# Performance work log

Measured on AMD Instinct MI355X. Metric: run time of the kernel, lower is better.

Reference implementation:

```python
import jax, jax.numpy as jnp
import numpy as np

DIM = 1024
NUM_HEADS = 16
DIM_PER_HEAD = 64
INNER = NUM_HEADS * DIM_PER_HEAD  # 1024
SCALE = DIM_PER_HEAD ** -0.5
EPS = 1e-10


def setup_inputs() -> dict:
    key = jax.random.key(0)
    k_x, k_m, k_qkv, k_wo, k_bo = jax.random.split(key, 5)
    b, l = 2, 2048
    x = jax.random.normal(k_x, (b, l, DIM), dtype=jnp.float32)
    # binary multiplicative mask [b, l, l]
    mask = jax.random.randint(k_m, (b, l, l), 0, 2).astype(jnp.float32)
    # nn.Linear(dim, 3*inner, bias=False): weight [3*inner, dim]; we store transposed [dim, 3*inner]
    W_qkv = jax.random.normal(k_qkv, (DIM, 3 * INNER), dtype=jnp.float32) * (DIM ** -0.5)
    W_out = jax.random.normal(k_wo, (INNER, DIM), dtype=jnp.float32) * (INNER ** -0.5)
    b_out = jax.random.normal(k_bo, (DIM,), dtype=jnp.float32) * 0.01
    return {"x": x, "mask": mask, "W_qkv": W_qkv, "W_out": W_out, "b_out": b_out}


def reference(x, mask, W_qkv, W_out, b_out):
    b, l, d = x.shape
    qkv = x @ W_qkv  # [b, l, 3*inner]
    qkv = qkv.reshape(b, l, 3, NUM_HEADS, DIM_PER_HEAD)
    qkv = jnp.transpose(qkv, (2, 0, 3, 1, 4))  # [3, b, h, l, dh]
    q, k, v = qkv[0], qkv[1], qkv[2]
    # softmax FIRST (no additive mask), matching the original module
    attn = jax.nn.softmax(jnp.einsum('bhid,bhjd->bhij', q, k) * SCALE, axis=-1)  # [b,h,l,l]
    # multiplicative mask then renormalize
    attn = attn * mask[:, None, :, :]
    attn = attn / (jnp.sum(attn, axis=-1, keepdims=True) + EPS)
    z = jnp.einsum('bhij,bhjd->bhid', attn, v)  # [b,h,l,dh]
    z = jnp.transpose(z, (0, 2, 1, 3)).reshape(b, l, INNER)
    out = z @ W_out + b_out  # dropout p=0 -> identity
    return out
```

## Files before the change

### kernel.cpp

```cpp
#include <hip/hip_runtime.h>
#include <hip/hip_bf16.h>

#define BATCH 2
#define SEQ   2048
#define DIM   1024
#define HEADS 16
#define DH    64
#define N_QKV 3072
#define M_TOT 4096
#define SCALE 0.125f
#define EPS   1e-10f
#define LOG2E 1.442695041f

typedef __attribute__((ext_vector_type(8))) _Float16 half8;
typedef __attribute__((ext_vector_type(4))) float f32x4;

static __device__ __forceinline__ unsigned short f2h(float f) {
    _Float16 h = (_Float16)f;
    return __builtin_bit_cast(unsigned short, h);
}
static __device__ __forceinline__ unsigned int pkrtz(float a, float b) {
#if defined(__has_builtin) && __has_builtin(__builtin_amdgcn_cvt_pkrtz)
    return __builtin_bit_cast(unsigned int, __builtin_amdgcn_cvt_pkrtz(a, b));
#else
    return (unsigned int)f2h(a) | ((unsigned int)f2h(b) << 16);
#endif
}
static __device__ __forceinline__ void glds16(const void* g, void* l) {
    __builtin_amdgcn_global_load_lds((const __attribute__((address_space(1))) void*)g,
                                     (__attribute__((address_space(3))) void*)l,
                                     16, 0, 0);
}

__global__ __launch_bounds__(256) void prepass(const float* __restrict__ x,
                                               unsigned short* __restrict__ xh,
                                               const float* __restrict__ Wq,
                                               unsigned short* __restrict__ WqT,
                                               const float* __restrict__ Wo,
                                               unsigned short* __restrict__ WoT,
                                               const float* __restrict__ mask,
                                               unsigned short* __restrict__ mbits) {
    const int bid = blockIdx.x;
    const int t   = threadIdx.x;
    __shared__ float tile[32][33];
    __shared__ unsigned char flags[16][256];

    if (bid < 4096) {
        const int i = bid * 256 + t;
        float4 v = reinterpret_cast<const float4*>(x)[i];
        uint2 o;
        o.x = pkrtz(v.x, v.y);
        o.y = pkrtz(v.z, v.w);
        reinterpret_cast<uint2*>(xh)[i] = o;
    } else if (bid < 8192) {
        const float* src; unsigned short* th; int rows, cols, bx;
        if (bid < 7168) { src = Wq; th = WqT; rows = 1024; cols = 3072; bx = bid - 4096;
        } else          { src = Wo; th = WoT; rows = 1024; cols = 1024; bx = bid - 7168; }
        const int nbx = cols / 32;
        const int c0 = (bx % nbx) * 32, r0 = (bx / nbx) * 32;
        const int tx = t & 31, ty = t >> 5;
        #pragma unroll
        for (int i = ty; i < 32; i += 8)
            tile[i][tx] = src[(long)(r0 + i) * cols + c0 + tx];
        __syncthreads();
        #pragma unroll
        for (int i = ty; i < 32; i += 8)
            th[(long)(c0 + i) * rows + r0 + tx] = f2h(tile[tx][i]);
    } else {
        const int bx = bid - 8192;
        const int it = bx & 127;
        const int bb = bx >> 7;
        const int R0 = it * 16;
        const int tl = t >> 6, ln = t & 63;
        for (int c0 = 0; c0 < SEQ; c0 += 256) {
            #pragma unroll
            for (int rr = 0; rr < 16; ++rr)
                flags[rr][t] = mask[((long)bb * SEQ + R0 + rr) * SEQ + c0 + t] != 0.f;
            __syncthreads();
            unsigned int bits = 0;
            #pragma unroll
            for (int nt = 0; nt < 4; ++nt)
                #pragma unroll
                for (int r = 0; r < 4; ++r)
                    bits |= (unsigned int)flags[ln & 15][tl * 64 + nt * 16 + ((ln >> 4) << 2) + r]
                            << (nt * 4 + r);
            mbits[(((long)bb * 128 + it) * 32 + (c0 >> 6) + tl) * 64 + ln] = (unsigned short)bits;
            __syncthreads();
        }
    }
}

__global__ __launch_bounds__(256, 3) void gemm_qkv_f16(
    const unsigned short* __restrict__ Ahg, const unsigned short* __restrict__ Bhg,
    unsigned short* __restrict__ qb, unsigned short* __restrict__ kb,
    unsigned short* __restrict__ vtb) {
    __shared__ __align__(16) unsigned short As[128 * 64];
    __shared__ __align__(16) unsigned short Bs[128 * 64];

    const int n0   = blockIdx.x * 128;
    const int m0   = blockIdx.y * 128;
    const int wave = threadIdx.x >> 6;
    const int lane = threadIdx.x & 63;
    const int l16  = lane & 15;
    const int g    = lane >> 4;
    const int wm   = wave & 1;
    const int wn   = wave >> 1;
    const int sw   = l16 & 7;

    const int sr8 = lane >> 3;
    const int scg = (lane & 7) ^ sr8;

    f32x4 acc[4][4] = {};

    for (int k0 = 0; k0 < DIM; k0 += 64) {
        #pragma unroll
        for (int i = 0; i < 4; ++i) {
            const int row = wave * 32 + i * 8;
            glds16(Ahg + (long)(m0 + row + sr8) * DIM + k0 + scg * 8, &As[row * 64]);
            glds16(Bhg + (long)(n0 + row + sr8) * DIM + k0 + scg * 8, &Bs[row * 64]);
        }
        __syncthreads();

        #pragma unroll
        for (int kc = 0; kc < 2; ++kc) {
            half8 a[4], b[4];
            #pragma unroll
            for (int mt = 0; mt < 4; ++mt)
                a[mt] = *reinterpret_cast<const half8*>(
                    &As[(wm * 64 + mt * 16 + l16) * 64 + (((kc * 4 + g) ^ sw) * 8)]);
            #pragma unroll
            for (int nt = 0; nt < 4; ++nt)
                b[nt] = *reinterpret_cast<const half8*>(
                    &Bs[(wn * 64 + nt * 16 + l16) * 64 + (((kc * 4 + g) ^ sw) * 8)]);
            #pragma unroll
            for (int mt = 0; mt < 4; ++mt)
                #pragma unroll
                for (int nt = 0; nt < 4; ++nt)
                    acc[mt][nt] = __builtin_amdgcn_mfma_f32_16x16x32_f16(
                        a[mt], b[nt], acc[mt][nt], 0, 0, 0);
        }
        __syncthreads();
    }

    #pragma unroll
    for (int nt = 0; nt < 4; ++nt) {
        const int n     = n0 + wn * 64 + nt * 16 + l16;
        const int which = n >> 10;
        const int rem   = n & 1023;
        const int head  = rem >> 6;
        const int d     = rem & 63;
        #pragma unroll
        for (int mt = 0; mt < 4; ++mt) {
            #pragma unroll
            for (int r = 0; r < 4; ++r) {
                const int m  = m0 + wm * 64 + mt * 16 + g * 4 + r;
                const int bb = m >> 11;
                const int li = m & 2047;
                const int bh_i = bb * HEADS + head;
                const float val = acc[mt][nt][r];
                if (which == 0)
                    qb[((long)bh_i * SEQ + li) * DH + d] = f2h(val * (SCALE * LOG2E));
                else if (which == 1)
                    kb[((long)bh_i * SEQ + li) * DH + d] = f2h(val);
                else
                    vtb[((long)bh_i * DH + d) * SEQ + li] = f2h(val);
            }
        }
    }
}

__global__ __launch_bounds__(256, 4) void gemm_out_f16(
    const unsigned short* __restrict__ Ahg, const unsigned short* __restrict__ Bhg,
    const float* __restrict__ bias, float* __restrict__ out) {
    __shared__ __align__(16) unsigned short As[64 * 64];
    __shared__ __align__(16) unsigned short Bs[64 * 64];

    const int n0   = blockIdx.x * 64;
    const int m0   = blockIdx.y * 64;
    const int wave = threadIdx.x >> 6;
    const int lane = threadIdx.x & 63;
    const int l16  = lane & 15;
    const int g    = lane >> 4;
    const int wm   = wave & 1;
    const int wn   = wave >> 1;
    const int sw   = l16 & 7;

    const int sr8 = lane >> 3;
    const int scg = (lane & 7) ^ sr8;

    f32x4 acc[2][2] = {};

    for (int k0 = 0; k0 < DIM; k0 += 64) {
        #pragma unroll
        for (int i = 0; i < 2; ++i) {
            const int row = wave * 16 + i * 8;
            glds16(Ahg + (long)(m0 + row + sr8) * DIM + k0 + scg * 8, &As[row * 64]);
            glds16(Bhg + (long)(n0 + row + sr8) * DIM + k0 + scg * 8, &Bs[row * 64]);
        }
        __syncthreads();

        half8 a[2][2];
        #pragma unroll
        for (int mt = 0; mt < 2; ++mt) {
            const int rbase = (wm * 32 + mt * 16 + l16) * 64;
            #pragma unroll
            for (int kc = 0; kc < 2; ++kc)
                a[mt][kc] = *reinterpret_cast<const half8*>(
                    &As[rbase + (((kc * 4 + g) ^ sw) * 8)]);
        }
        #pragma unroll
        for (int nt = 0; nt < 2; ++nt) {
            const int rbase = (wn * 32 + nt * 16 + l16) * 64;
            const half8 b0 = *reinterpret_cast<const half8*>(&Bs[rbase + (((0 + g) ^ sw) * 8)]);
            const half8 b1 = *reinterpret_cast<const half8*>(&Bs[rbase + (((4 + g) ^ sw) * 8)]);
            #pragma unroll
            for (int mt = 0; mt < 2; ++mt) {
                acc[mt][nt] = __builtin_amdgcn_mfma_f32_16x16x32_f16(a[mt][0], b0, acc[mt][nt], 0, 0, 0);
                acc[mt][nt] = __builtin_amdgcn_mfma_f32_16x16x32_f16(a[mt][1], b1, acc[mt][nt], 0, 0, 0);
            }
        }
        __syncthreads();
    }

    #pragma unroll
    for (int nt = 0; nt < 2; ++nt) {
        const int n  = n0 + wn * 32 + nt * 16 + l16;
        const float bv = bias[n];
        #pragma unroll
        for (int mt = 0; mt < 2; ++mt) {
            #pragma unroll
            for (int r = 0; r < 4; ++r) {
                const int m = m0 + wm * 32 + mt * 16 + g * 4 + r;
                out[(long)m * DIM + n] = acc[mt][nt][r] + bv;
            }
        }
    }
}

__global__ __launch_bounds__(512, 6) void attn_mfma(const unsigned short* __restrict__ qb,
                                                    const unsigned short* __restrict__ kb,
                                                    const unsigned short* __restrict__ vtb,
                                                    const unsigned short* __restrict__ mbits,
                                                    unsigned short* __restrict__ zh) {
    const int qt   = blockIdx.x;
    const int h    = blockIdx.y;
    const int bb   = blockIdx.z;
    const int bh   = bb * HEADS + h;
    const int wave = threadIdx.x >> 6;
    const int lane = threadIdx.x & 63;
    const int l16  = lane & 15;
    const int g    = lane >> 4;
    const int wm   = wave >> 1;
    const int wj   = wave & 1;

    const int myrow0 = qt * 64 + wm * 16;

    __shared__ __align__(16) unsigned short KV[2][2][64 * 64];
    __shared__ __align__(16) unsigned short Ps[8][16 * 64];

    const int sr8 = lane >> 3;
    const int scg = (lane & 7) ^ sr8;
    const int sw  = l16 & 7;

    const unsigned short* qptr = qb + ((long)bh * SEQ + myrow0 + l16) * DH + g * 8;
    const half8 q0 = *reinterpret_cast<const half8*>(qptr);
    const half8 q1 = *reinterpret_cast<const half8*>(qptr + 32);

    half8 ones;
    #pragma unroll
    for (int j = 0; j < 8; ++j) ones[j] = (_Float16)1.0f;

    f32x4 o[4] = {};
    f32x4 oz = {0.f, 0.f, 0.f, 0.f};

    const unsigned short* mb =
        mbits + (((long)bb * 128 + qt * 4 + wm) * 32 + wj * 16) * 64 + lane;
    const long kbase = (long)bh * SEQ * DH;
    const long vbase = (long)bh * DH * SEQ;
    const int  jb    = wj * 1024;

    for (int it = 0; it < 16; ++it) {
        const int j0 = jb + it * 64;
        const unsigned int bits = mb[(long)it * 64];

        #pragma unroll
        for (int i = 0; i < 2; ++i) {
            const int row = wm * 16 + i * 8;
            glds16(kb  + kbase + (long)(j0 + row + sr8) * DH + scg * 8, &KV[wj][0][row * 64]);
            glds16(vtb + vbase + (long)(row + sr8) * SEQ + j0 + scg * 8, &KV[wj][1][row * 64]);
        }
        __syncthreads();

        f32x4 st[4];
        #pragma unroll
        for (int nt = 0; nt < 4; ++nt) {
            const int rbase = (nt * 16 + l16) * 64;
            const half8 k0 = *reinterpret_cast<const half8*>(&KV[wj][0][rbase + ((0 + g) ^ sw) * 8]);
            const half8 k1 = *reinterpret_cast<const half8*>(&KV[wj][0][rbase + (((4 + g) ^ sw) * 8)]);
            f32x4 acc = {0.f, 0.f, 0.f, 0.f};
            acc = __builtin_amdgcn_mfma_f32_16x16x32_f16(k0, q0, acc, 0, 0, 0);
            acc = __builtin_amdgcn_mfma_f32_16x16x32_f16(k1, q1, acc, 0, 0, 0);
            st[nt] = acc;
        }

        #pragma unroll
        for (int nt = 0; nt < 4; ++nt) {
            float pm[4];
            #pragma unroll
            for (int r = 0; r < 4; ++r) {
                const float p = __builtin_amdgcn_exp2f(st[nt][r]);
                pm[r] = ((bits >> (nt * 4 + r)) & 1u) ? p : 0.f;
            }
            uint2 pk;
            pk.x = pkrtz(pm[0], pm[1]);
            pk.y = pkrtz(pm[2], pm[3]);
            *reinterpret_cast<uint2*>(
                &Ps[wave][l16 * 64 + (((2 * nt + (g >> 1)) ^ sw) * 8) + (g & 1) * 4]) = pk;
        }

        const half8 pb0 = *reinterpret_cast<const half8*>(&Ps[wave][l16 * 64 + ((0 + g) ^ sw) * 8]);
        const half8 pb1 = *reinterpret_cast<const half8*>(&Ps[wave][l16 * 64 + (((4 + g) ^ sw) * 8)]);
        #pragma unroll
        for (int dt = 0; dt < 4; ++dt) {
            const int vb = (dt * 16 + l16) * 64;
            const half8 v0 = *reinterpret_cast<const half8*>(&KV[wj][1][vb + ((0 + g) ^ sw) * 8]);
            const half8 v1 = *reinterpret_cast<const half8*>(&KV[wj][1][vb + (((4 + g) ^ sw) * 8)]);
            o[dt] = __builtin_amdgcn_mfma_f32_16x16x32_f16(v0, pb0, o[dt], 0, 0, 0);
            o[dt] = __builtin_amdgcn_mfma_f32_16x16x32_f16(v1, pb1, o[dt], 0, 0, 0);
        }
        oz = __builtin_amdgcn_mfma_f32_16x16x32_f16(ones, pb0, oz, 0, 0, 0);
        oz = __builtin_amdgcn_mfma_f32_16x16x32_f16(ones, pb1, oz, 0, 0, 0);
        __syncthreads();
    }

    float* cmb = (float*)&KV[0][0][0];
    const int ci = wm * 16 + l16;
    if (wj == 1) {
        #pragma unroll
        for (int dt = 0; dt < 4; ++dt)
            *reinterpret_cast<f32x4*>(&cmb[ci * 68 + dt * 16 + g * 4]) = o[dt];
        if (g == 0) cmb[4352 + ci] = oz[0];
    }
    __syncthreads();
    if (wj == 0) {
        const float Z   = oz[0] + cmb[4352 + ci];
        const float inv = 1.f / (Z + 1e-30f);
        const long obase = ((long)bb * SEQ + myrow0 + l16) * DIM + h * DH;
        #pragma unroll
        for (int dt = 0; dt < 4; ++dt) {
            const f32x4 oc = *reinterpret_cast<const f32x4*>(&cmb[ci * 68 + dt * 16 + g * 4]);
            uint2 pk;
            pk.x = pkrtz((o[dt][0] + oc[0]) * inv, (o[dt][1] + oc[1]) * inv);
            pk.y = pkrtz((o[dt][2] + oc[2]) * inv, (o[dt][3] + oc[3]) * inv);
            *reinterpret_cast<uint2*>(zh + obase + dt * 16 + g * 4) = pk;
        }
    }
}

extern "C" void kernel_launch(void* const* d_in, const int* in_sizes, int n_in,
                              void* d_out, int out_size, void* d_ws, size_t ws_size,
                              hipStream_t stream) {
    const float* x     = (const float*)d_in[0];
    const float* mask  = (const float*)d_in[1];
    const float* W_qkv = (const float*)d_in[2];
    const float* W_out = (const float*)d_in[3];
    const float* b_out = (const float*)d_in[4];
    float* out = (float*)d_out;

    unsigned short* ws = (unsigned short*)d_ws;
    unsigned short* xh    = ws;
    unsigned short* WqT   = xh    + 4194304;
    unsigned short* WoT   = WqT   + 3145728;
    unsigned short* qbu   = WoT   + 1048576;
    unsigned short* kbu   = qbu   + 4194304;
    unsigned short* vtb   = kbu   + 4194304;
    unsigned short* mbits = vtb   + 4194304;
    unsigned short* zz    = xh;

    prepass<<<8448, 256, 0, stream>>>(x, xh, W_qkv, WqT, W_out, WoT, mask, mbits);

    gemm_qkv_f16<<<dim3(24, 32), 256, 0, stream>>>(xh, WqT, qbu, kbu, vtb);

    attn_mfma<<<dim3(SEQ / 64, HEADS, BATCH), 512, 0, stream>>>(qbu, kbu, vtb, mbits, zz);

    gemm_out_f16<<<dim3(16, 64), 256, 0, stream>>>(zz, WoT, b_out, out);
}
```

Baseline: 229.4 us.

## Process 128 query rows per attention block to reuse K/V tiles

The attention kernel now handles 128 query rows per block instead of 64. Each wave computes two 16-row query sub-tiles against the same K/V tiles loaded into shared memory, which halves global K/V traffic and the number of barriers per query row. The cost is more registers per wave (the launch-bounds occupancy hint drops from 6 to 4), a larger shared memory footprint, and half as many blocks in the grid.

```diff
diff --git a/kernel.cpp b/kernel.cpp
--- a/kernel.cpp
+++ b/kernel.cpp
@@ -237,7 +237,7 @@
     }
 }
 
-__global__ __launch_bounds__(512, 6) void attn_mfma(const unsigned short* __restrict__ qb,
+__global__ __launch_bounds__(512, 4) void attn_mfma(const unsigned short* __restrict__ qb,
                                                     const unsigned short* __restrict__ kb,
                                                     const unsigned short* __restrict__ vtb,
                                                     const unsigned short* __restrict__ mbits,
@@ -253,106 +253,138 @@
     const int wm   = wave >> 1;
     const int wj   = wave & 1;
 
-    const int myrow0 = qt * 64 + wm * 16;
-
-    __shared__ __align__(16) unsigned short KV[2][2][64 * 64];
-    __shared__ __align__(16) unsigned short Ps[8][16 * 64];
+    const int myrow0 = qt * 128 + wm * 32;
+
+    __shared__ __align__(16) unsigned short shm[32768];
 
     const int sr8 = lane >> 3;
     const int scg = (lane & 7) ^ sr8;
     const int sw  = l16 & 7;
 
+    unsigned short* Ks = &shm[wj * 8192];
+    unsigned short* Vs = &shm[wj * 8192 + 4096];
+    unsigned short* P0 = &shm[16384 + wave * 1024];
+    unsigned short* P1 = &shm[24576 + wave * 1024];
+
     const unsigned short* qptr = qb + ((long)bh * SEQ + myrow0 + l16) * DH + g * 8;
     const half8 q0 = *reinterpret_cast<const half8*>(qptr);
     const half8 q1 = *reinterpret_cast<const half8*>(qptr + 32);
+    const half8 q2 = *reinterpret_cast<const half8*>(qptr + 16 * DH);
+    const half8 q3 = *reinterpret_cast<const half8*>(qptr + 16 * DH + 32);
 
     half8 ones;
     #pragma unroll
     for (int j = 0; j < 8; ++j) ones[j] = (_Float16)1.0f;
 
-    f32x4 o[4] = {};
-    f32x4 oz = {0.f, 0.f, 0.f, 0.f};
+    f32x4 o0[4] = {}, o1[4] = {};
+    f32x4 oz0 = {0.f, 0.f, 0.f, 0.f};
+    f32x4 oz1 = {0.f, 0.f, 0.f, 0.f};
 
     const unsigned short* mb =
-        mbits + (((long)bb * 128 + qt * 4 + wm) * 32 + wj * 16) * 64 + lane;
+        mbits + (((long)bb * 128 + qt * 8 + wm * 2) * 32 + wj * 16) * 64 + lane;
     const long kbase = (long)bh * SEQ * DH;
     const long vbase = (long)bh * DH * SEQ;
     const int  jb    = wj * 1024;
 
     for (int it = 0; it < 16; ++it) {
         const int j0 = jb + it * 64;
-        const unsigned int bits = mb[(long)it * 64];
+        const unsigned int bits0 = mb[(long)it * 64];
+        const unsigned int bits1 = mb[(long)it * 64 + 2048];
 
         #pragma unroll
         for (int i = 0; i < 2; ++i) {
             const int row = wm * 16 + i * 8;
-            glds16(kb  + kbase + (long)(j0 + row + sr8) * DH + scg * 8, &KV[wj][0][row * 64]);
-            glds16(vtb + vbase + (long)(row + sr8) * SEQ + j0 + scg * 8, &KV[wj][1][row * 64]);
-        }
-        __syncthreads();
-
-        f32x4 st[4];
+            glds16(kb  + kbase + (long)(j0 + row + sr8) * DH + scg * 8, Ks + row * 64);
+            glds16(vtb + vbase + (long)(row + sr8) * SEQ + j0 + scg * 8, Vs + row * 64);
+        }
+        __syncthreads();
+
         #pragma unroll
         for (int nt = 0; nt < 4; ++nt) {
             const int rbase = (nt * 16 + l16) * 64;
-            const half8 k0 = *reinterpret_cast<const half8*>(&KV[wj][0][rbase + ((0 + g) ^ sw) * 8]);
-            const half8 k1 = *reinterpret_cast<const half8*>(&KV[wj][0][rbase + (((4 + g) ^ sw) * 8)]);
-            f32x4 acc = {0.f, 0.f, 0.f, 0.f};
-            acc = __builtin_amdgcn_mfma_f32_16x16x32_f16(k0, q0, acc, 0, 0, 0);
-            acc = __builtin_amdgcn_mfma_f32_16x16x32_f16(k1, q1, acc, 0, 0, 0);
-            st[nt] = acc;
-        }
-
-        #pragma unroll
-        for (int nt = 0; nt < 4; ++nt) {
-            float pm[4];
+            const half8 k0 = *reinterpret_cast<const half8*>(&Ks[rbase + ((0 + g) ^ sw) * 8]);
+            const half8 k1 = *reinterpret_cast<const half8*>(&Ks[rbase + (((4 + g) ^ sw) * 8)]);
+            f32x4 s0 = {0.f, 0.f, 0.f, 0.f};
+            f32x4 s1 = {0.f, 0.f, 0.f, 0.f};
+            s0 = __builtin_amdgcn_mfma_f32_16x16x32_f16(k0, q0, s0, 0, 0, 0);
+            s0 = __builtin_amdgcn_mfma_f32_16x16x32_f16(k1, q1, s0, 0, 0, 0);
+            s1 = __builtin_amdgcn_mfma_f32_16x16x32_f16(k0, q2, s1, 0, 0, 0);
+            s1 = __builtin_amdgcn_mfma_f32_16x16x32_f16(k1, q3, s1, 0, 0, 0);
+
+            float pa[4], pb[4];
             #pragma unroll
             for (int r = 0; r < 4; ++r) {
-                const float p = __builtin_amdgcn_exp2f(st[nt][r]);
-                pm[r] = ((bits >> (nt * 4 + r)) & 1u) ? p : 0.f;
+                const float e0 = __builtin_amdgcn_exp2f(s0[r]);
+                const float e1 = __builtin_amdgcn_exp2f(s1[r]);
+                pa[r] = ((bits0 >> (nt * 4 + r)) & 1u) ? e0 : 0.f;
+                pb[r] = ((bits1 >> (nt * 4 + r)) & 1u) ? e1 : 0.f;
             }
-            uint2 pk;
-            pk.x = pkrtz(pm[0], pm[1]);
-            pk.y = pkrtz(pm[2], pm[3]);
-            *reinterpret_cast<uint2*>(
-                &Ps[wave][l16 * 64 + (((2 * nt + (g >> 1)) ^ sw) * 8) + (g & 1) * 4]) = pk;
-        }
-
-        const half8 pb0 = *reinterpret_cast<const half8*>(&Ps[wave][l16 * 64 + ((0 + g) ^ sw) * 8]);
-        const half8 pb1 = *reinterpret_cast<const half8*>(&Ps[wave][l16 * 64 + (((4 + g) ^ sw) * 8)]);
+            const int poff = l16 * 64 + (((2 * nt + (g >> 1)) ^ sw) * 8) + (g & 1) * 4;
+            uint2 pk0, pk1;
+            pk0.x = pkrtz(pa[0], pa[1]);
+            pk0.y = pkrtz(pa[2], pa[3]);
+            pk1.x = pkrtz(pb[0], pb[1]);
+            pk1.y = pkrtz(pb[2], pb[3]);
+            *reinterpret_cast<uint2*>(&P0[poff]) = pk0;
+            *reinterpret_cast<uint2*>(&P1[poff]) = pk1;
+        }
+
+        const half8 pb00 = *reinterpret_cast<const half8*>(&P0[l16 * 64 + ((0 + g) ^ sw) * 8]);
+        const half8 pb01 = *reinterpret_cast<const half8*>(&P0[l16 * 64 + (((4 + g) ^ sw) * 8)]);
+        const half8 pb10 = *reinterpret_cast<const half8*>(&P1[l16 * 64 + ((0 + g) ^ sw) * 8]);
+        const half8 pb11 = *reinterpret_cast<const half8*>(&P1[l16 * 64 + (((4 + g) ^ sw) * 8)]);
+
         #pragma unroll
         for (int dt = 0; dt < 4; ++dt) {
             const int vb = (dt * 16 + l16) * 64;
-            const half8 v0 = *reinterpret_cast<const half8*>(&KV[wj][1][vb + ((0 + g) ^ sw) * 8]);
-            const half8 v1 = *reinterpret_cast<const half8*>(&KV[wj][1][vb + (((4 + g) ^ sw) * 8)]);
-            o[dt] = __builtin_amdgcn_mfma_f32_16x16x32_f16(v0, pb0, o[dt], 0, 0, 0);
-            o[dt] = __builtin_amdgcn_mfma_f32_16x16x32_f16(v1, pb1, o[dt], 0, 0, 0);
-        }
-        oz = __builtin_amdgcn_mfma_f32_16x16x32_f16(ones, pb0, oz, 0, 0, 0);
-        oz = __builtin_amdgcn_mfma_f32_16x16x32_f16(ones, pb1, oz, 0, 0, 0);
-        __syncthreads();
-    }
-
-    float* cmb = (float*)&KV[0][0][0];
-    const int ci = wm * 16 + l16;
+            const half8 v0 = *reinterpret_cast<const half8*>(&Vs[vb + ((0 + g) ^ sw) * 8]);
+            const half8 v1 = *reinterpret_cast<const half8*>(&Vs[vb + (((4 + g) ^ sw) * 8)]);
+            o0[dt] = __builtin_amdgcn_mfma_f32_16x16x32_f16(v0, pb00, o0[dt], 0, 0, 0);
+            o0[dt] = __builtin_amdgcn_mfma_f32_16x16x32_f16(v1, pb01, o0[dt], 0, 0, 0);
+            o1[dt] = __builtin_amdgcn_mfma_f32_16x16x32_f16(v0, pb10, o1[dt], 0, 0, 0);
+            o1[dt] = __builtin_amdgcn_mfma_f32_16x16x32_f16(v1, pb11, o1[dt], 0, 0, 0);
+        }
+        oz0 = __builtin_amdgcn_mfma_f32_16x16x32_f16(ones, pb00, oz0, 0, 0, 0);
+        oz0 = __builtin_amdgcn_mfma_f32_16x16x32_f16(ones, pb01, oz0, 0, 0, 0);
+        oz1 = __builtin_amdgcn_mfma_f32_16x16x32_f16(ones, pb10, oz1, 0, 0, 0);
+        oz1 = __builtin_amdgcn_mfma_f32_16x16x32_f16(ones, pb11, oz1, 0, 0, 0);
+        __syncthreads();
+    }
+
+    float* cmb = (float*)shm;
+    const int ZOFF = 128 * 68;
+    const int ci0  = wm * 32 + l16;
+    const int ci1  = ci0 + 16;
     if (wj == 1) {
         #pragma unroll
-        for (int dt = 0; dt < 4; ++dt)
-            *reinterpret_cast<f32x4*>(&cmb[ci * 68 + dt * 16 + g * 4]) = o[dt];
-        if (g == 0) cmb[4352 + ci] = oz[0];
+        for (int dt = 0; dt < 4; ++dt) {
+            *reinterpret_cast<f32x4*>(&cmb[ci0 * 68 + dt * 16 + g * 4]) = o0[dt];
+            *reinterpret_cast<f32x4*>(&cmb[ci1 * 68 + dt * 16 + g * 4]) = o1[dt];
+        }
+        if (g == 0) {
+            cmb[ZOFF + ci0] = oz0[0];
+            cmb[ZOFF + ci1] = oz1[0];
+        }
     }
     __syncthreads();
     if (wj == 0) {
-        const float Z   = oz[0] + cmb[4352 + ci];
-        const float inv = 1.f / (Z + 1e-30f);
-        const long obase = ((long)bb * SEQ + myrow0 + l16) * DIM + h * DH;
+        const float Z0   = oz0[0] + cmb[ZOFF + ci0];
+        const float Z1   = oz1[0] + cmb[ZOFF + ci1];
+        const float inv0 = 1.f / (Z0 + 1e-30f);
+        const float inv1 = 1.f / (Z1 + 1e-30f);
+        const long obase0 = ((long)bb * SEQ + myrow0 + l16) * DIM + h * DH;
+        const long obase1 = obase0 + (long)16 * DIM;
         #pragma unroll
         for (int dt = 0; dt < 4; ++dt) {
-            const f32x4 oc = *reinterpret_cast<const f32x4*>(&cmb[ci * 68 + dt * 16 + g * 4]);
+            const f32x4 oc0 = *reinterpret_cast<const f32x4*>(&cmb[ci0 * 68 + dt * 16 + g * 4]);
+            const f32x4 oc1 = *reinterpret_cast<const f32x4*>(&cmb[ci1 * 68 + dt * 16 + g * 4]);
             uint2 pk;
-            pk.x = pkrtz((o[dt][0] + oc[0]) * inv, (o[dt][1] + oc[1]) * inv);
-            pk.y = pkrtz((o[dt][2] + oc[2]) * inv, (o[dt][3] + oc[3]) * inv);
-            *reinterpret_cast<uint2*>(zh + obase + dt * 16 + g * 4) = pk;
+            pk.x = pkrtz((o0[dt][0] + oc0[0]) * inv0, (o0[dt][1] + oc0[1]) * inv0);
+            pk.y = pkrtz((o0[dt][2] + oc0[2]) * inv0, (o0[dt][3] + oc0[3]) * inv0);
+            *reinterpret_cast<uint2*>(zh + obase0 + dt * 16 + g * 4) = pk;
+            pk.x = pkrtz((o1[dt][0] + oc1[0]) * inv1, (o1[dt][1] + oc1[1]) * inv1);
+            pk.y = pkrtz((o1[dt][2] + oc1[2]) * inv1, (o1[dt][3] + oc1[3]) * inv1);
+            *reinterpret_cast<uint2*>(zh + obase1 + dt * 16 + g * 4) = pk;
         }
     }
 }
@@ -381,7 +413,7 @@
 
     gemm_qkv_f16<<<dim3(24, 32), 256, 0, stream>>>(xh, WqT, qbu, kbu, vtb);
 
-    attn_mfma<<<dim3(SEQ / 64, HEADS, BATCH), 512, 0, stream>>>(qbu, kbu, vtb, mbits, zz);
+    attn_mfma<<<dim3(SEQ / 128, HEADS, BATCH), 512, 0, stream>>>(qbu, kbu, vtb, mbits, zz);
 
     gemm_out_f16<<<dim3(16, 64), 256, 0, stream>>>(zz, WoT, b_out, out);
 }
```

After: 229.9 us. About the same (+0.2%).
